# Kernel tuning notes

Hardware: AMD Instinct MI355X
Metric: run time of the kernel (lower is better)

Reference implementation:

```python
import jax, jax.numpy as jnp
import numpy as np
from jax import lax

B, C, H, W = 8, 256, 128, 128
O = 256
KH, KW = 1, 3
PH, PW = 0, 1
K = KH * KW


def setup_inputs() -> dict:
    key = jax.random.key(0)
    k1, k2, k3, k4 = jax.random.split(key, 4)
    x = jax.random.normal(k1, (B, C, H, W), jnp.float32)
    # offset-predicting conv (small init so sample points stay near the grid)
    offset_w = jax.random.normal(k2, (2 * K, C, KH, KW), jnp.float32) * 0.01
    offset_b = jax.random.normal(k3, (2 * K,), jnp.float32) * 0.01
    # deformable conv weight, no bias (bias=False in the module)
    deform_w = jax.random.normal(k4, (O, C, KH, KW), jnp.float32) * (1.0 / np.sqrt(C * K))
    return {"x": x, "offset_w": offset_w, "offset_b": offset_b, "deform_w": deform_w}


def _gather_corner(x_flat, yi, xi, valid_dtype):
    # x_flat: [B, C, H*W]; yi, xi: int32 [B, K, Ho, Wo]
    valid = (yi >= 0) & (yi < H) & (xi >= 0) & (xi < W)
    yc = jnp.clip(yi, 0, H - 1)
    xc = jnp.clip(xi, 0, W - 1)
    idx = yc * W + xc  # [B, K, Ho, Wo]
    # per-batch fancy gather -> [B, C, K, Ho, Wo]
    g = jax.vmap(lambda f, i: f[:, i])(x_flat, idx)
    return g * valid[:, None].astype(valid_dtype)


def _deform_conv(x, offset, deform_w):
    # torchvision-style deform_conv2d with zero padding, groups=1, dg=1
    Ho, Wo = offset.shape[2], offset.shape[3]
    off = offset.reshape(B, K, 2, Ho, Wo)
    off_y, off_x = off[:, :, 0], off[:, :, 1]  # [B, K, Ho, Wo]

    k = jnp.arange(K)
    base_y = (-PH + (k // KW)).astype(x.dtype)[None, :, None, None]
    base_x = (-PW + (k % KW)).astype(x.dtype)[None, :, None, None]
    grid_y = jnp.arange(Ho, dtype=x.dtype)[None, None, :, None]
    grid_x = jnp.arange(Wo, dtype=x.dtype)[None, None, None, :]

    py = grid_y + base_y + off_y  # fractional sample rows [B,K,Ho,Wo]
    px = grid_x + base_x + off_x  # fractional sample cols

    y0f = jnp.floor(py)
    x0f = jnp.floor(px)
    wy = (py - y0f)[:, None]  # [B,1,K,Ho,Wo]
    wx = (px - x0f)[:, None]
    y0 = y0f.astype(jnp.int32)
    x0 = x0f.astype(jnp.int32)
    y1 = y0 + 1
    x1 = x0 + 1

    x_flat = x.reshape(B, C, H * W)
    v00 = _gather_corner(x_flat, y0, x0, x.dtype)
    v01 = _gather_corner(x_flat, y0, x1, x.dtype)
    v10 = _gather_corner(x_flat, y1, x0, x.dtype)
    v11 = _gather_corner(x_flat, y1, x1, x.dtype)

    sampled = (v00 * (1 - wy) * (1 - wx) + v01 * (1 - wy) * wx
               + v10 * wy * (1 - wx) + v11 * wy * wx)  # [B,C,K,Ho,Wo]

    return jnp.einsum('bckhw,ock->bohw', sampled, deform_w.reshape(O, C, K))


def reference(x, offset_w, offset_b, deform_w):
    # offset conv (stride 1, padding (0,1))
    offset = lax.conv_general_dilated(x, offset_w, window_strides=(1, 1),
                                      padding=[(PH, PH), (PW, PW)])
    offset = offset + offset_b[None, :, None, None]
    # in-place zeroing from the original forward
    offset = offset.at[:, 1].set(0.0).at[:, 4].set(0.0)
    return _deform_conv(x, offset, deform_w)
```

## Files before the change

### kernel.cpp

```cpp
#include <hip/hip_runtime.h>
#include <hip/hip_bf16.h>

#define Bn 8
#define Cn 256
#define Hn 128
#define Wn 128
#define On 256
#define HWn (Hn*Wn)
#define Pn  HWn
#define Rpad 896
#define W2ROW 768
#define QC  ((size_t)Pn * Cn)

typedef __attribute__((ext_vector_type(8))) short bf16x8;
typedef __attribute__((ext_vector_type(4))) float f32x4;

__device__ __forceinline__ void gload_lds16(const void* g, void* l) {
  __builtin_amdgcn_global_load_lds(
      (__attribute__((address_space(1))) void*)g,
      (__attribute__((address_space(3))) void*)l, 16, 0, 0);
}

__device__ __forceinline__ unsigned short f2bf(float f) {
  unsigned int u = __float_as_uint(f);
  unsigned int r = (u + 0x7fffu + ((u >> 16) & 1u)) >> 16;
  return (unsigned short)r;
}
__device__ __forceinline__ float bf2f(unsigned short u) {
  return __uint_as_float(((unsigned int)u) << 16);
}
__device__ __forceinline__ void bacc(uint4 v, float w, float* f) {
  f[0] += w * __uint_as_float(v.x << 16);
  f[1] += w * __uint_as_float(v.x & 0xffff0000u);
  f[2] += w * __uint_as_float(v.y << 16);
  f[3] += w * __uint_as_float(v.y & 0xffff0000u);
  f[4] += w * __uint_as_float(v.z << 16);
  f[5] += w * __uint_as_float(v.z & 0xffff0000u);
  f[6] += w * __uint_as_float(v.w << 16);
  f[7] += w * __uint_as_float(v.w & 0xffff0000u);
}

__global__ __launch_bounds__(256) void k_wprep(
    const float* __restrict__ dw, const float* __restrict__ ow,
    unsigned short* __restrict__ W2, unsigned short* __restrict__ Wbig) {
  int r = blockIdx.x;
  int c = threadIdx.x;
  float v = 0.f;
  if (r < 768) {
    int k = r >> 8, o = r & 255;
    v = dw[((size_t)o * Cn + c) * 3 + k];
    W2[(size_t)o * W2ROW + k * 256 + c] = f2bf(v);
  } else if (r < 786) {
    int rr = r - 768;
    int oc = rr / 3, kw = rr - 3 * oc;
    v = ow[((size_t)oc * Cn + c) * 3 + kw];
  }
  Wbig[(size_t)r * Cn + c] = f2bf(v);
}

__global__ __launch_bounds__(256) void k_transpose(
    const float* __restrict__ x, unsigned short* __restrict__ xbT) {
  int b = blockIdx.z;
  int q0 = blockIdx.x * 64, c0 = blockIdx.y * 64;
  __shared__ unsigned short t[64][66];
  int tid = threadIdx.x;
  int qi = tid & 63, cg = tid >> 6;
  const float* xb = x + (size_t)b * Cn * HWn;
  #pragma unroll
  for (int i = 0; i < 16; ++i) {
    int cl = i * 4 + cg;
    t[cl][qi] = f2bf(xb[(size_t)(c0 + cl) * HWn + q0 + qi]);
  }
  __syncthreads();
  unsigned short* dst = xbT + (size_t)b * QC;
  int c2 = (tid & 31) * 2, qg = tid >> 5;
  #pragma unroll
  for (int j = 0; j < 8; ++j) {
    int ql = j * 8 + qg;
    unsigned int u = (unsigned int)t[c2][ql] | ((unsigned int)t[c2 + 1][ql] << 16);
    *(unsigned int*)(dst + (size_t)(q0 + ql) * Cn + c0 + c2) = u;
  }
}

__global__ __launch_bounds__(256) void k_goff(
    const unsigned short* __restrict__ xbT,
    const unsigned short* __restrict__ Wbig,
    unsigned short* __restrict__ Goff) {
  int q0 = blockIdx.y * 128;
  const unsigned short* xb = xbT + (size_t)blockIdx.z * QC;
  unsigned short* Gz = Goff + (size_t)blockIdx.z * Pn * 32;
  __shared__ unsigned short Qs[128 * 64];
  __shared__ unsigned short Ws[128 * 64];
  int tid = threadIdx.x;
  int lane = tid & 63, wid = tid >> 6;
  int wr = wid >> 1, wc = wid & 1;
  f32x4 acc[4][4];
  #pragma unroll
  for (int m = 0; m < 4; ++m)
    #pragma unroll
    for (int n = 0; n < 4; ++n) acc[m][n] = (f32x4){0.f, 0.f, 0.f, 0.f};

  for (int kt = 0; kt < 4; ++kt) {
    int ck0 = kt * 64;
    __syncthreads();
    #pragma unroll
    for (int i = 0; i < 4; ++i) {
      int fo = wid * 1024 + i * 4096 + lane * 16;
      int row = fo >> 7;
      int slot = (fo >> 4) & 7;
      int ss = slot ^ (row & 7);
      gload_lds16(xb   + (size_t)(q0 + row) * Cn + ck0 + ss * 8, (char*)Qs + fo);
      gload_lds16(Wbig + (size_t)(768 + row) * Cn + ck0 + ss * 8, (char*)Ws + fo);
    }
    __syncthreads();
    #pragma unroll
    for (int s = 0; s < 2; ++s) {
      bf16x8 af[4], bfr[4];
      #pragma unroll
      for (int m = 0; m < 4; ++m) {
        int row = wr * 64 + m * 16 + (lane & 15);
        int slot = (s * 4 + (lane >> 4)) ^ (row & 7);
        af[m] = *(const bf16x8*)((const char*)Qs + row * 128 + slot * 16);
      }
      #pragma unroll
      for (int n = 0; n < 4; ++n) {
        int row = wc * 64 + n * 16 + (lane & 15);
        int slot = (s * 4 + (lane >> 4)) ^ (row & 7);
        bfr[n] = *(const bf16x8*)((const char*)Ws + row * 128 + slot * 16);
      }
      #pragma unroll
      for (int m = 0; m < 4; ++m)
        #pragma unroll
        for (int n = 0; n < 4; ++n)
          acc[m][n] = __builtin_amdgcn_mfma_f32_16x16x32_bf16(af[m], bfr[n], acc[m][n], 0, 0, 0);
    }
  }
  if (wc == 0) {
    #pragma unroll
    for (int m = 0; m < 4; ++m)
      #pragma unroll
      for (int n = 0; n < 2; ++n)
        #pragma unroll
        for (int rr = 0; rr < 4; ++rr) {
          int q = q0 + wr * 64 + m * 16 + (lane >> 4) * 4 + rr;
          int j = n * 16 + (lane & 15);
          if (j < 18) Gz[(size_t)q * 32 + j] = f2bf(acc[m][n][rr]);
        }
  }
}

__global__ __launch_bounds__(512) void k_fgemm(
    const unsigned short* __restrict__ xbT,
    const unsigned short* __restrict__ W2,
    const unsigned short* __restrict__ Goff,
    const float* __restrict__ obias,
    float* __restrict__ out) {
  int pt = blockIdx.x, z = blockIdx.y;
  int ho = (pt & 7) * 16 + (pt >> 3);
  const unsigned short* xz = xbT + (size_t)z * QC;
  const unsigned short* Gf = Goff + (size_t)z * Pn * 32;

  __shared__ unsigned short Qs[256 * 64];
  __shared__ unsigned short Ss[128 * 64];
  __shared__ float Sw4[128][3][4];
  __shared__ int   Sq4[128][3][4];

  int tid = threadIdx.x;
  if (tid < 384) {
    int k = tid >> 7;
    int wo = tid & 127;
    float offy = 0.f, offx = 0.f;
    int ocy = 2 * k, ocx = 2 * k + 1;
    if (ocy != 4) {
      float s = obias[ocy];
      #pragma unroll
      for (int kw = 0; kw < 3; ++kw) {
        int col = wo + kw - 1;
        if (col >= 0 && col < Wn)
          s += bf2f(Gf[(size_t)(ho * Wn + col) * 32 + ocy * 3 + kw]);
      }
      offy = s;
    }
    if (ocx != 1) {
      float s = obias[ocx];
      #pragma unroll
      for (int kw = 0; kw < 3; ++kw) {
        int col = wo + kw - 1;
        if (col >= 0 && col < Wn)
          s += bf2f(Gf[(size_t)(ho * Wn + col) * 32 + ocx * 3 + kw]);
      }
      offx = s;
    }
    float py = (float)ho + offy;
    float px = (float)(wo + k - 1) + offx;
    float y0f = floorf(py), x0f = floorf(px);
    float wy = py - y0f, wx = px - x0f;
    int y0 = (int)y0f, x0 = (int)x0f;
    int y1 = y0 + 1, x1 = x0 + 1;
    bool vy0 = (y0 >= 0) && (y0 < Hn), vy1 = (y1 >= 0) && (y1 < Hn);
    bool vx0 = (x0 >= 0) && (x0 < Wn), vx1 = (x1 >= 0) && (x1 < Wn);
    int yc0 = min(max(y0, 0), Hn - 1), yc1 = min(max(y1, 0), Hn - 1);
    int xc0 = min(max(x0, 0), Wn - 1), xc1 = min(max(x1, 0), Wn - 1);
    Sq4[wo][k][0] = (yc0 * Wn + xc0) * 512;
    Sq4[wo][k][1] = (yc0 * Wn + xc1) * 512;
    Sq4[wo][k][2] = (yc1 * Wn + xc0) * 512;
    Sq4[wo][k][3] = (yc1 * Wn + xc1) * 512;
    Sw4[wo][k][0] = (vy0 && vx0) ? (1.f - wy) * (1.f - wx) : 0.f;
    Sw4[wo][k][1] = (vy0 && vx1) ? (1.f - wy) * wx : 0.f;
    Sw4[wo][k][2] = (vy1 && vx0) ? wy * (1.f - wx) : 0.f;
    Sw4[wo][k][3] = (vy1 && vx1) ? wy * wx : 0.f;
  }

  int lane = tid & 63, wid = tid >> 6;
  int wr = wid >> 1, wc = wid & 1;
  int oct = tid & 7, pg = tid >> 3;
  f32x4 acc[4][4];
  #pragma unroll
  for (int m = 0; m < 4; ++m)
    #pragma unroll
    for (int n = 0; n < 4; ++n) acc[m][n] = (f32x4){0.f, 0.f, 0.f, 0.f};

  __syncthreads();

  for (int kt = 0; kt < 12; ++kt) {
    int k = kt >> 2;
    int c0 = (kt & 3) << 6;
    __syncthreads();
    #pragma unroll
    for (int i = 0; i < 4; ++i) {
      int t = tid + i * 512;
      int fo = t << 4;
      int row = fo >> 7;
      int slot = (fo >> 4) & 7;
      int ss = slot ^ (row & 7);
      gload_lds16(W2 + (size_t)row * W2ROW + k * 256 + c0 + ss * 8, (char*)Qs + fo);
    }
    const char* bse = (const char*)xz + (c0 + oct * 8) * 2;
    #pragma unroll
    for (int i = 0; i < 2; ++i) {
      int pl = pg + 64 * i;
      float w0 = Sw4[pl][k][0], w1 = Sw4[pl][k][1], w2 = Sw4[pl][k][2], w3 = Sw4[pl][k][3];
      uint4 v0 = *(const uint4*)(bse + Sq4[pl][k][0]);
      uint4 v1 = *(const uint4*)(bse + Sq4[pl][k][1]);
      uint4 v2 = *(const uint4*)(bse + Sq4[pl][k][2]);
      uint4 v3 = *(const uint4*)(bse + Sq4[pl][k][3]);
      float f[8] = {0.f, 0.f, 0.f, 0.f, 0.f, 0.f, 0.f, 0.f};
      bacc(v0, w0, f); bacc(v1, w1, f); bacc(v2, w2, f); bacc(v3, w3, f);
      uint4 r;
      r.x = (unsigned int)f2bf(f[0]) | ((unsigned int)f2bf(f[1]) << 16);
      r.y = (unsigned int)f2bf(f[2]) | ((unsigned int)f2bf(f[3]) << 16);
      r.z = (unsigned int)f2bf(f[4]) | ((unsigned int)f2bf(f[5]) << 16);
      r.w = (unsigned int)f2bf(f[6]) | ((unsigned int)f2bf(f[7]) << 16);
      *(uint4*)((char*)Ss + pl * 128 + ((oct ^ (pl & 7)) << 4)) = r;
    }
    __syncthreads();
    #pragma unroll
    for (int s = 0; s < 2; ++s) {
      bf16x8 af[4], bfr[4];
      #pragma unroll
      for (int m = 0; m < 4; ++m) {
        int row = wr * 64 + m * 16 + (lane & 15);
        int slot = (s * 4 + (lane >> 4)) ^ (row & 7);
        af[m] = *(const bf16x8*)((const char*)Qs + row * 128 + slot * 16);
      }
      #pragma unroll
      for (int n = 0; n < 4; ++n) {
        int row = wc * 64 + n * 16 + (lane & 15);
        int slot = (s * 4 + (lane >> 4)) ^ (row & 7);
        bfr[n] = *(const bf16x8*)((const char*)Ss + row * 128 + slot * 16);
      }
      #pragma unroll
      for (int m = 0; m < 4; ++m)
        #pragma unroll
        for (int n = 0; n < 4; ++n)
          acc[m][n] = __builtin_amdgcn_mfma_f32_16x16x32_bf16(af[m], bfr[n], acc[m][n], 0, 0, 0);
    }
  }
  float* ob_ = out + (size_t)z * On * Pn + (size_t)ho * Wn;
  #pragma unroll
  for (int m = 0; m < 4; ++m)
    #pragma unroll
    for (int n = 0; n < 4; ++n)
      #pragma unroll
      for (int rr = 0; rr < 4; ++rr) {
        int o = wr * 64 + m * 16 + (lane >> 4) * 4 + rr;
        int pc = wc * 64 + n * 16 + (lane & 15);
        ob_[(size_t)o * Pn + pc] = acc[m][n][rr];
      }
}

extern "C" void kernel_launch(void* const* d_in, const int* in_sizes, int n_in,
                              void* d_out, int out_size, void* d_ws, size_t ws_size,
                              hipStream_t stream) {
  const float* x  = (const float*)d_in[0];
  const float* ow = (const float*)d_in[1];
  const float* ob = (const float*)d_in[2];
  const float* dw = (const float*)d_in[3];
  float* out = (float*)d_out;

  char* ws = (char*)d_ws;
  size_t w2_bytes   = (size_t)On * W2ROW * 2;
  size_t wbig_bytes = (size_t)Rpad * Cn * 2;
  size_t xbT_bytes  = QC * 2;
  size_t w2_al   = (w2_bytes + 255) & ~(size_t)255;
  size_t wbig_al = (wbig_bytes + 255) & ~(size_t)255;

  unsigned short* W2   = (unsigned short*)ws;
  unsigned short* Wbig = (unsigned short*)(ws + w2_al);
  unsigned short* xbT  = (unsigned short*)(ws + w2_al + wbig_al);
  unsigned short* Goff = (unsigned short*)(ws + w2_al + wbig_al + (size_t)Bn * xbT_bytes);
  (void)ws_size;

  k_wprep<<<Rpad, 256, 0, stream>>>(dw, ow, W2, Wbig);
  k_transpose<<<dim3(256, 4, Bn), 256, 0, stream>>>(x, xbT);
  k_goff<<<dim3(1, 128, Bn), 256, 0, stream>>>(xbT, Wbig, Goff);
  k_fgemm<<<dim3(128, Bn), 512, 0, stream>>>(xbT, W2, Goff, ob, out);
}
```

Before: 184.0 us.

## Software-pipeline deformable gather with double-buffered LDS and direct-global weight loads

Rewrites the main GEMM loop of the fused deformable-conv kernel as a fully unrolled 12-step software pipeline. The bilinear corner gathers are issued two steps ahead into registers, the sample tile is double-buffered in LDS so one barrier per step suffices, and the weight tile (W2) is read straight from global memory into MFMA A fragments instead of being staged through LDS. This aims to hide gather latency behind the MFMAs and halve barrier count. The cost is higher register pressure (prefetch buffers, precomputed offsets, A fragments) and uncoalesced, repeated global reads of weights.

```diff
diff --git a/kernel.cpp b/kernel.cpp
--- a/kernel.cpp
+++ b/kernel.cpp
@@ -160,8 +160,7 @@
   const unsigned short* xz = xbT + (size_t)z * QC;
   const unsigned short* Gf = Goff + (size_t)z * Pn * 32;
 
-  __shared__ unsigned short Qs[256 * 64];
-  __shared__ unsigned short Ss[128 * 64];
+  __shared__ unsigned short Ss[2][128 * 64];
   __shared__ float Sw4[128][3][4];
   __shared__ int   Sq4[128][3][4];
 
@@ -212,8 +211,10 @@
   }
 
   int lane = tid & 63, wid = tid >> 6;
+  int lg = lane >> 4;
   int wr = wid >> 1, wc = wid & 1;
   int oct = tid & 7, pg = tid >> 3;
+  int plA = pg, plB = pg + 64;
   f32x4 acc[4][4];
   #pragma unroll
   for (int m = 0; m < 4; ++m)
@@ -222,60 +223,114 @@
 
   __syncthreads();
 
-  for (int kt = 0; kt < 12; ++kt) {
-    int k = kt >> 2;
-    int c0 = (kt & 3) << 6;
-    __syncthreads();
-    #pragma unroll
-    for (int i = 0; i < 4; ++i) {
-      int t = tid + i * 512;
-      int fo = t << 4;
-      int row = fo >> 7;
-      int slot = (fo >> 4) & 7;
-      int ss = slot ^ (row & 7);
-      gload_lds16(W2 + (size_t)row * W2ROW + k * 256 + c0 + ss * 8, (char*)Qs + fo);
-    }
-    const char* bse = (const char*)xz + (c0 + oct * 8) * 2;
-    #pragma unroll
-    for (int i = 0; i < 2; ++i) {
-      int pl = pg + 64 * i;
-      float w0 = Sw4[pl][k][0], w1 = Sw4[pl][k][1], w2 = Sw4[pl][k][2], w3 = Sw4[pl][k][3];
-      uint4 v0 = *(const uint4*)(bse + Sq4[pl][k][0]);
-      uint4 v1 = *(const uint4*)(bse + Sq4[pl][k][1]);
-      uint4 v2 = *(const uint4*)(bse + Sq4[pl][k][2]);
-      uint4 v3 = *(const uint4*)(bse + Sq4[pl][k][3]);
-      float f[8] = {0.f, 0.f, 0.f, 0.f, 0.f, 0.f, 0.f, 0.f};
-      bacc(v0, w0, f); bacc(v1, w1, f); bacc(v2, w2, f); bacc(v3, w3, f);
-      uint4 r;
-      r.x = (unsigned int)f2bf(f[0]) | ((unsigned int)f2bf(f[1]) << 16);
-      r.y = (unsigned int)f2bf(f[2]) | ((unsigned int)f2bf(f[3]) << 16);
-      r.z = (unsigned int)f2bf(f[4]) | ((unsigned int)f2bf(f[5]) << 16);
-      r.w = (unsigned int)f2bf(f[6]) | ((unsigned int)f2bf(f[7]) << 16);
-      *(uint4*)((char*)Ss + pl * 128 + ((oct ^ (pl & 7)) << 4)) = r;
-    }
-    __syncthreads();
-    #pragma unroll
-    for (int s = 0; s < 2; ++s) {
-      bf16x8 af[4], bfr[4];
-      #pragma unroll
-      for (int m = 0; m < 4; ++m) {
-        int row = wr * 64 + m * 16 + (lane & 15);
-        int slot = (s * 4 + (lane >> 4)) ^ (row & 7);
-        af[m] = *(const bf16x8*)((const char*)Qs + row * 128 + slot * 16);
-      }
-      #pragma unroll
-      for (int n = 0; n < 4; ++n) {
-        int row = wc * 64 + n * 16 + (lane & 15);
-        int slot = (s * 4 + (lane >> 4)) ^ (row & 7);
-        bfr[n] = *(const bf16x8*)((const char*)Ss + row * 128 + slot * 16);
-      }
-      #pragma unroll
-      for (int m = 0; m < 4; ++m)
-        #pragma unroll
-        for (int n = 0; n < 4; ++n)
-          acc[m][n] = __builtin_amdgcn_mfma_f32_16x16x32_bf16(af[m], bfr[n], acc[m][n], 0, 0, 0);
-    }
-  }
+  int qr[3][8];
+  #pragma unroll
+  for (int k = 0; k < 3; ++k)
+    #pragma unroll
+    for (int c = 0; c < 4; ++c) {
+      qr[k][c]     = Sq4[plA][k][c] + oct * 16;
+      qr[k][4 + c] = Sq4[plB][k][c] + oct * 16;
+    }
+  const char* xzb = (const char*)xz;
+  const char* w2p[4];
+  #pragma unroll
+  for (int m = 0; m < 4; ++m)
+    w2p[m] = (const char*)W2 + (size_t)(wr * 64 + m * 16 + (lane & 15)) * (W2ROW * 2) + lg * 16;
+  char* SsB = (char*)Ss;
+  int dsA = plA * 128 + ((oct ^ (plA & 7)) << 4);
+  int dsB = plB * 128 + ((oct ^ (plB & 7)) << 4);
+
+  uint4 gs[2][8];
+
+  #pragma unroll
+  for (int i = 0; i < 8; ++i) gs[0][i] = *(const uint4*)(xzb + qr[0][i]);
+  #pragma unroll
+  for (int i = 0; i < 8; ++i) gs[1][i] = *(const uint4*)(xzb + qr[0][i] + 128);
+  {
+    float4 w4a = *(const float4*)&Sw4[plA][0][0];
+    float4 w4b = *(const float4*)&Sw4[plB][0][0];
+    float fA[8] = {0,0,0,0,0,0,0,0}, fB[8] = {0,0,0,0,0,0,0,0};
+    bacc(gs[0][0], w4a.x, fA); bacc(gs[0][1], w4a.y, fA); bacc(gs[0][2], w4a.z, fA); bacc(gs[0][3], w4a.w, fA);
+    bacc(gs[0][4], w4b.x, fB); bacc(gs[0][5], w4b.y, fB); bacc(gs[0][6], w4b.z, fB); bacc(gs[0][7], w4b.w, fB);
+    uint4 rA, rB;
+    rA.x = f2bf(fA[0]) | ((unsigned)f2bf(fA[1]) << 16); rA.y = f2bf(fA[2]) | ((unsigned)f2bf(fA[3]) << 16);
+    rA.z = f2bf(fA[4]) | ((unsigned)f2bf(fA[5]) << 16); rA.w = f2bf(fA[6]) | ((unsigned)f2bf(fA[7]) << 16);
+    rB.x = f2bf(fB[0]) | ((unsigned)f2bf(fB[1]) << 16); rB.y = f2bf(fB[2]) | ((unsigned)f2bf(fB[3]) << 16);
+    rB.z = f2bf(fB[4]) | ((unsigned)f2bf(fB[5]) << 16); rB.w = f2bf(fB[6]) | ((unsigned)f2bf(fB[7]) << 16);
+    *(uint4*)(SsB + dsA) = rA;
+    *(uint4*)(SsB + dsB) = rB;
+  }
+  asm volatile("s_waitcnt lgkmcnt(0)" ::: "memory");
+  __builtin_amdgcn_sched_barrier(0);
+  __builtin_amdgcn_s_barrier();
+  __builtin_amdgcn_sched_barrier(0);
+  asm volatile("" ::: "memory");
+
+#define FBODY(T) do {                                                          \
+                               \
+    bf16x8 a_[2][4];                                                           \
+    _Pragma("unroll")                                                          \
+    for (int s = 0; s < 2; ++s)                                                \
+      _Pragma("unroll")                                                        \
+      for (int m = 0; m < 4; ++m)                                              \
+        a_[s][m] = *(const bf16x8*)(w2p[m] + ((T) >> 2) * 512 + ((T) & 3) * 128 + s * 64); \
+                                                          \
+    if ((T) < 10) {                                                            \
+      _Pragma("unroll")                                                        \
+      for (int i = 0; i < 8; ++i)                                              \
+        gs[(T) & 1][i] = *(const uint4*)(xzb + qr[((T) + 2) >> 2][i] + (((T) + 2) & 3) * 128); \
+    }                                                                          \
+                                          \
+    if ((T) < 11) {                                                            \
+      float4 w4a = *(const float4*)&Sw4[plA][((T) + 1) >> 2][0];               \
+      float4 w4b = *(const float4*)&Sw4[plB][((T) + 1) >> 2][0];               \
+      float fA[8] = {0,0,0,0,0,0,0,0}, fB[8] = {0,0,0,0,0,0,0,0};              \
+      bacc(gs[((T)+1)&1][0], w4a.x, fA); bacc(gs[((T)+1)&1][1], w4a.y, fA);    \
+      bacc(gs[((T)+1)&1][2], w4a.z, fA); bacc(gs[((T)+1)&1][3], w4a.w, fA);    \
+      bacc(gs[((T)+1)&1][4], w4b.x, fB); bacc(gs[((T)+1)&1][5], w4b.y, fB);    \
+      bacc(gs[((T)+1)&1][6], w4b.z, fB); bacc(gs[((T)+1)&1][7], w4b.w, fB);    \
+      uint4 rA, rB;                                                            \
+      rA.x = f2bf(fA[0]) | ((unsigned)f2bf(fA[1]) << 16);                      \
+      rA.y = f2bf(fA[2]) | ((unsigned)f2bf(fA[3]) << 16);                      \
+      rA.z = f2bf(fA[4]) | ((unsigned)f2bf(fA[5]) << 16);                      \
+      rA.w = f2bf(fA[6]) | ((unsigned)f2bf(fA[7]) << 16);                      \
+      rB.x = f2bf(fB[0]) | ((unsigned)f2bf(fB[1]) << 16);                      \
+      rB.y = f2bf(fB[2]) | ((unsigned)f2bf(fB[3]) << 16);                      \
+      rB.z = f2bf(fB[4]) | ((unsigned)f2bf(fB[5]) << 16);                      \
+      rB.w = f2bf(fB[6]) | ((unsigned)f2bf(fB[7]) << 16);                      \
+      *(uint4*)(SsB + (((T) + 1) & 1) * 16384 + dsA) = rA;                     \
+      *(uint4*)(SsB + (((T) + 1) & 1) * 16384 + dsB) = rB;                     \
+    }                                                                          \
+                                              \
+    _Pragma("unroll")                                                          \
+    for (int s = 0; s < 2; ++s) {                                              \
+      bf16x8 b_[4];                                                            \
+      _Pragma("unroll")                                                        \
+      for (int n = 0; n < 4; ++n) {                                            \
+        int row = wc * 64 + n * 16 + (lane & 15);                              \
+        int slot = (s * 4 + lg) ^ (row & 7);                                   \
+        b_[n] = *(const bf16x8*)(SsB + ((T) & 1) * 16384 + row * 128 + slot * 16); \
+      }                                                                        \
+      _Pragma("unroll")                                                        \
+      for (int m = 0; m < 4; ++m)                                              \
+        _Pragma("unroll")                                                      \
+        for (int n = 0; n < 4; ++n)                                            \
+          acc[m][n] = __builtin_amdgcn_mfma_f32_16x16x32_bf16(a_[s][m], b_[n], acc[m][n], 0, 0, 0); \
+    }                                                                          \
+    if ((T) < 11) {                                                            \
+      asm volatile("s_waitcnt lgkmcnt(0)" ::: "memory");                       \
+      __builtin_amdgcn_sched_barrier(0);                                       \
+      __builtin_amdgcn_s_barrier();                                            \
+      __builtin_amdgcn_sched_barrier(0);                                       \
+      asm volatile("" ::: "memory");                                           \
+    }                                                                          \
+  } while (0)
+
+  FBODY(0);  FBODY(1);  FBODY(2);  FBODY(3);
+  FBODY(4);  FBODY(5);  FBODY(6);  FBODY(7);
+  FBODY(8);  FBODY(9);  FBODY(10); FBODY(11);
+#undef FBODY
+
   float* ob_ = out + (size_t)z * On * Pn + (size_t)ho * Wn;
   #pragma unroll
   for (int m = 0; m < 4; ++m)
@@ -283,7 +338,7 @@
     for (int n = 0; n < 4; ++n)
       #pragma unroll
       for (int rr = 0; rr < 4; ++rr) {
-        int o = wr * 64 + m * 16 + (lane >> 4) * 4 + rr;
+        int o = wr * 64 + m * 16 + lg * 4 + rr;
         int pc = wc * 64 + n * 16 + (lane & 15);
         ob_[(size_t)o * Pn + pc] = acc[m][n][rr];
       }
```

After: 213.2 us. 1.16x slower.

## Prefetch next K-tile bilinear gathers into registers during MFMA compute

Applied to the files above, without the earlier changes.

The gather of the four bilinear corner values for the next K-tile is issued right after the barrier, so global load latency overlaps the MFMA inner loop instead of sitting on the critical path before it. Sampling weights are loaded as float4, and the k-loop is fully unrolled. s_setprio raises wave priority around the MFMA section. The cost is eight extra uint4 registers plus weights held live across compute, which adds register pressure and may lower occupancy.

```diff
diff --git a/kernel.cpp b/kernel.cpp
--- a/kernel.cpp
+++ b/kernel.cpp
@@ -212,8 +212,10 @@
   }
 
   int lane = tid & 63, wid = tid >> 6;
+  int lg = lane >> 4;
   int wr = wid >> 1, wc = wid & 1;
   int oct = tid & 7, pg = tid >> 3;
+  int plA = pg, plB = pg + 64;
   f32x4 acc[4][4];
   #pragma unroll
   for (int m = 0; m < 4; ++m)
@@ -222,6 +224,32 @@
 
   __syncthreads();
 
+  const char* xzb = (const char*)xz;
+  int octo = oct * 16;
+  int dsA = plA * 128 + ((oct ^ (plA & 7)) << 4);
+  int dsB = plB * 128 + ((oct ^ (plB & 7)) << 4);
+
+  uint4 gA0, gA1, gA2, gA3, gB0, gB1, gB2, gB3;
+  float4 w4a, w4b;
+
+  #define PREF(KT) do {                                                        \
+    int kk = (KT) >> 2, cc = ((KT) & 3) << 7;   \
+    w4a = *(const float4*)&Sw4[plA][kk][0];                                    \
+    w4b = *(const float4*)&Sw4[plB][kk][0];                                    \
+    const char* bse = xzb + cc + octo;                                         \
+    gA0 = *(const uint4*)(bse + Sq4[plA][kk][0]);                              \
+    gA1 = *(const uint4*)(bse + Sq4[plA][kk][1]);                              \
+    gA2 = *(const uint4*)(bse + Sq4[plA][kk][2]);                              \
+    gA3 = *(const uint4*)(bse + Sq4[plA][kk][3]);                              \
+    gB0 = *(const uint4*)(bse + Sq4[plB][kk][0]);                              \
+    gB1 = *(const uint4*)(bse + Sq4[plB][kk][1]);                              \
+    gB2 = *(const uint4*)(bse + Sq4[plB][kk][2]);                              \
+    gB3 = *(const uint4*)(bse + Sq4[plB][kk][3]);                              \
+  } while (0)
+
+  PREF(0);
+
+  #pragma unroll
   for (int kt = 0; kt < 12; ++kt) {
     int k = kt >> 2;
     int c0 = (kt & 3) << 6;
@@ -235,38 +263,42 @@
       int ss = slot ^ (row & 7);
       gload_lds16(W2 + (size_t)row * W2ROW + k * 256 + c0 + ss * 8, (char*)Qs + fo);
     }
-    const char* bse = (const char*)xz + (c0 + oct * 8) * 2;
-    #pragma unroll
-    for (int i = 0; i < 2; ++i) {
-      int pl = pg + 64 * i;
-      float w0 = Sw4[pl][k][0], w1 = Sw4[pl][k][1], w2 = Sw4[pl][k][2], w3 = Sw4[pl][k][3];
-      uint4 v0 = *(const uint4*)(bse + Sq4[pl][k][0]);
-      uint4 v1 = *(const uint4*)(bse + Sq4[pl][k][1]);
-      uint4 v2 = *(const uint4*)(bse + Sq4[pl][k][2]);
-      uint4 v3 = *(const uint4*)(bse + Sq4[pl][k][3]);
+    {
       float f[8] = {0.f, 0.f, 0.f, 0.f, 0.f, 0.f, 0.f, 0.f};
-      bacc(v0, w0, f); bacc(v1, w1, f); bacc(v2, w2, f); bacc(v3, w3, f);
+      bacc(gA0, w4a.x, f); bacc(gA1, w4a.y, f); bacc(gA2, w4a.z, f); bacc(gA3, w4a.w, f);
       uint4 r;
-      r.x = (unsigned int)f2bf(f[0]) | ((unsigned int)f2bf(f[1]) << 16);
-      r.y = (unsigned int)f2bf(f[2]) | ((unsigned int)f2bf(f[3]) << 16);
-      r.z = (unsigned int)f2bf(f[4]) | ((unsigned int)f2bf(f[5]) << 16);
-      r.w = (unsigned int)f2bf(f[6]) | ((unsigned int)f2bf(f[7]) << 16);
-      *(uint4*)((char*)Ss + pl * 128 + ((oct ^ (pl & 7)) << 4)) = r;
+      r.x = (unsigned)f2bf(f[0]) | ((unsigned)f2bf(f[1]) << 16);
+      r.y = (unsigned)f2bf(f[2]) | ((unsigned)f2bf(f[3]) << 16);
+      r.z = (unsigned)f2bf(f[4]) | ((unsigned)f2bf(f[5]) << 16);
+      r.w = (unsigned)f2bf(f[6]) | ((unsigned)f2bf(f[7]) << 16);
+      *(uint4*)((char*)Ss + dsA) = r;
+    }
+    {
+      float f[8] = {0.f, 0.f, 0.f, 0.f, 0.f, 0.f, 0.f, 0.f};
+      bacc(gB0, w4b.x, f); bacc(gB1, w4b.y, f); bacc(gB2, w4b.z, f); bacc(gB3, w4b.w, f);
+      uint4 r;
+      r.x = (unsigned)f2bf(f[0]) | ((unsigned)f2bf(f[1]) << 16);
+      r.y = (unsigned)f2bf(f[2]) | ((unsigned)f2bf(f[3]) << 16);
+      r.z = (unsigned)f2bf(f[4]) | ((unsigned)f2bf(f[5]) << 16);
+      r.w = (unsigned)f2bf(f[6]) | ((unsigned)f2bf(f[7]) << 16);
+      *(uint4*)((char*)Ss + dsB) = r;
     }
     __syncthreads();
+    if (kt < 11) PREF(kt + 1);
+    __builtin_amdgcn_s_setprio(1);
     #pragma unroll
     for (int s = 0; s < 2; ++s) {
       bf16x8 af[4], bfr[4];
       #pragma unroll
       for (int m = 0; m < 4; ++m) {
         int row = wr * 64 + m * 16 + (lane & 15);
-        int slot = (s * 4 + (lane >> 4)) ^ (row & 7);
+        int slot = (s * 4 + lg) ^ (row & 7);
         af[m] = *(const bf16x8*)((const char*)Qs + row * 128 + slot * 16);
       }
       #pragma unroll
       for (int n = 0; n < 4; ++n) {
         int row = wc * 64 + n * 16 + (lane & 15);
-        int slot = (s * 4 + (lane >> 4)) ^ (row & 7);
+        int slot = (s * 4 + lg) ^ (row & 7);
         bfr[n] = *(const bf16x8*)((const char*)Ss + row * 128 + slot * 16);
       }
       #pragma unroll
@@ -275,7 +307,10 @@
         for (int n = 0; n < 4; ++n)
           acc[m][n] = __builtin_amdgcn_mfma_f32_16x16x32_bf16(af[m], bfr[n], acc[m][n], 0, 0, 0);
     }
-  }
+    __builtin_amdgcn_s_setprio(0);
+  }
+  #undef PREF
+
   float* ob_ = out + (size_t)z * On * Pn + (size_t)ho * Wn;
   #pragma unroll
   for (int m = 0; m < 4; ++m)
@@ -283,7 +318,7 @@
     for (int n = 0; n < 4; ++n)
       #pragma unroll
       for (int rr = 0; rr < 4; ++rr) {
-        int o = wr * 64 + m * 16 + (lane >> 4) * 4 + rr;
+        int o = wr * 64 + m * 16 + lg * 4 + rr;
         int pc = wc * 64 + n * 16 + (lane & 15);
         ob_[(size_t)o * Pn + pc] = acc[m][n][rr];
       }
```

Measured after the change: 183.2 us. No clear change (-0.4%).
